# Kernel optimization log

Hardware: AMD Instinct MI355X
Metric: run time of the kernel (lower is better)

## Reference

```python
import jax, jax.numpy as jnp
import numpy as np

N_QUBITS = 10
N_LAYERS = 4
DIM = 2 ** N_QUBITS


def _bit(v, q, n):
    return (v >> (n - 1 - q)) & 1


def _cnot_indices(control, target, n):
    idx0, idx1 = [], []
    for i in range(2 ** n):
        if _bit(i, control, n) == 1 and _bit(i, target, n) == 0:
            idx0.append(i)
            idx1.append(i | (1 << (n - 1 - target)))
    return np.asarray(idx0, np.int32), np.asarray(idx1, np.int32)


# static precomputed CNOT swap indices for pairs (q, (q+1) % n)
_CNOT = [_cnot_indices(q, (q + 1) % N_QUBITS, N_QUBITS) for q in range(N_QUBITS)]
# Z expectation masks: [n_qubits, dim] of +/-1
_ZMASK = np.array([[1.0 - 2.0 * _bit(i, q, N_QUBITS) for i in range(DIM)]
                   for q in range(N_QUBITS)], np.float32)


def _rx(t):
    c = jnp.cos(t / 2.0).astype(jnp.complex64)
    s = jnp.sin(t / 2.0).astype(jnp.complex64)
    return jnp.stack([jnp.stack([c, -1j * s], -1),
                      jnp.stack([-1j * s, c], -1)], -2)


def _ry(t):
    c = jnp.cos(t / 2.0).astype(jnp.complex64)
    s = jnp.sin(t / 2.0).astype(jnp.complex64)
    return jnp.stack([jnp.stack([c, -s], -1),
                      jnp.stack([s, c], -1)], -2)


def _rz(t):
    tc = t.astype(jnp.complex64)
    e0 = jnp.exp(-1j * tc / 2.0)
    e1 = jnp.exp(1j * tc / 2.0)
    z = jnp.zeros_like(e0)
    return jnp.stack([jnp.stack([e0, z], -1),
                      jnp.stack([z, e1], -1)], -2)


def _apply_gate(state, gate, q):
    # state: [b, DIM] complex64; gate: [2,2] or [b,2,2]
    b = state.shape[0]
    psi = state.reshape((b,) + (2,) * N_QUBITS)
    psi = jnp.moveaxis(psi, q + 1, N_QUBITS).reshape(b, DIM // 2, 2)
    if gate.ndim == 3:
        out = jnp.einsum('bmi,bij->bmj', psi, gate)
    else:
        out = jnp.einsum('bmi,ij->bmj', psi, gate)
    out = out.reshape((b,) + (2,) * N_QUBITS)
    out = jnp.moveaxis(out, N_QUBITS, q + 1)
    return out.reshape(b, DIM)


def _cnot(state, idx0, idx1):
    return state.at[:, idx0].set(state[:, idx1]).at[:, idx1].set(state[:, idx0])


def setup_inputs() -> dict:
    key = jax.random.key(0)
    k1, k2, k3, k4 = jax.random.split(key, 4)
    x = jax.random.normal(k1, (16384, 3), jnp.float32)
    enc_W = jax.random.normal(k2, (N_QUBITS, 3), jnp.float32) * 0.3
    enc_b = jax.random.normal(k3, (N_QUBITS,), jnp.float32) * 0.1
    theta = jax.random.normal(k4, (N_LAYERS, N_QUBITS, 3), jnp.float32) * 0.04
    return {"x": x, "enc_W": enc_W, "enc_b": enc_b, "theta": theta}


def reference(x, enc_W, enc_b, theta):
    b = x.shape[0]
    enc = jnp.pi * jnp.tanh(x @ enc_W.T + enc_b)  # [b, n_qubits]
    state = jnp.zeros((b, DIM), jnp.complex64).at[:, 0].set(1.0 + 0j)
    # batched encoding RY rotations
    for q in range(N_QUBITS):
        state = _apply_gate(state, _ry(enc[:, q]), q)
    # variational layers (shared gate across batch)
    for layer in range(N_LAYERS):
        for q in range(N_QUBITS):
            state = _apply_gate(state, _rx(theta[layer, q, 0]), q)
            state = _apply_gate(state, _ry(theta[layer, q, 1]), q)
            state = _apply_gate(state, _rz(theta[layer, q, 2]), q)
        for idx0, idx1 in _CNOT:
            state = _cnot(state, idx0, idx1)
    probs = jnp.square(state.real) + jnp.square(state.imag)  # [b, DIM]
    return probs @ jnp.asarray(_ZMASK).T  # [b, n_qubits]
```

## Files before the change

### kernel.cpp

```cpp
#include <hip/hip_runtime.h>
#include <stdint.h>

#define NQ 10
#define NL 4

typedef unsigned int u32;
typedef _Float16 f16x8 __attribute__((ext_vector_type(8)));
typedef float f32x16 __attribute__((ext_vector_type(16)));
typedef u32 u32x4 __attribute__((ext_vector_type(4)));

constexpr u32 FRc(u32 r) {
    u32 r0 = r & 1, r1 = (r >> 1) & 1, r2 = (r >> 2) & 1, r3 = (r >> 3) & 1, r4 = (r >> 4) & 1;
    return (r4 << 9) | ((r3 ^ r4) << 8) | ((r2 ^ r3) << 7) | ((r1 ^ r2) << 6) |
           ((r0 ^ r1) << 5) | (r0 << 4);
}
constexpr u32 FCc(u32 c) {
    u32 c0 = c & 1, c1 = (c >> 1) & 1, c2 = (c >> 2) & 1, c3 = (c >> 3) & 1, c4 = (c >> 4) & 1;
    return (c0 << 9) | (c0 << 8) | (c4 << 4) | ((c3 ^ c4) << 3) | ((c2 ^ c3) << 2) |
           ((c1 ^ c2) << 1) | (c0 ^ c1);
}
constexpr u32 FIr(u32 r) {
    u32 r0 = r & 1, r1 = (r >> 1) & 1, r2 = (r >> 2) & 1, r3 = (r >> 3) & 1, r4 = (r >> 4) & 1;
    u32 P = r0 ^ r1 ^ r2 ^ r3 ^ r4;
    return ((r0 ^ r1 ^ r2 ^ r3) << 9) | ((r3 ^ r4) << 8) | ((r2 ^ r3 ^ r4) << 7) |
           ((r1 ^ r2 ^ r3 ^ r4) << 6) | (P << 5) | (P << 4) | (P << 3) | (P << 2) | (P << 1) | P;
}
constexpr u32 FIcf(u32 c) {
    u32 c0 = c & 1, c1 = (c >> 1) & 1, c2 = (c >> 2) & 1, c3 = (c >> 3) & 1, c4 = (c >> 4) & 1;
    u32 Q = c0 ^ c1 ^ c2 ^ c3 ^ c4;
    return (Q << 9) | (c4 << 4) | ((c3 ^ c4) << 3) | ((c2 ^ c3 ^ c4) << 2) |
           ((c1 ^ c2 ^ c3 ^ c4) << 1) | Q;
}

__device__ __forceinline__ f32x16 mfma16(f16x8 a, f16x8 b, f32x16 c) {
    return __builtin_amdgcn_mfma_f32_32x32x16_f16(a, b, c, 0, 0, 0);
}
__device__ __forceinline__ f32x16 zero16() {
    f32x16 z;
#pragma unroll
    for (int i = 0; i < 16; i++) z[i] = 0.f;
    return z;
}
__device__ __forceinline__ f16x8 negf(f16x8 v) {
    u32x4 u = __builtin_bit_cast(u32x4, v);
#pragma unroll
    for (int i = 0; i < 4; i++) u[i] ^= 0x80008000u;
    return __builtin_bit_cast(f16x8, u);
}
__device__ __forceinline__ u32 pk2(float re, float im) {
    auto h = __builtin_amdgcn_cvt_pkrtz(re, im);
    return __builtin_bit_cast(u32, h);
}
__device__ __forceinline__ u32 permlo(u32 a, u32 b) {
    return __builtin_amdgcn_perm(b, a, 0x05040100u);
}
__device__ __forceinline__ u32 permhi(u32 a, u32 b) {
    return __builtin_amdgcn_perm(b, a, 0x07060302u);
}
__device__ __forceinline__ f16x8 mk8(u32 a, u32 b, u32 c, u32 d) {
    u32x4 v;
    v[0] = a; v[1] = b; v[2] = c; v[3] = d;
    return __builtin_bit_cast(f16x8, v);
}
template <int MASK>
__device__ __forceinline__ float swz(float v) {
    return __int_as_float(
        __builtin_amdgcn_ds_swizzle(__float_as_int(v), (MASK << 10) | 0x1F));
}
__device__ __forceinline__ float bperm(int addr, float v) {
    return __int_as_float(__builtin_amdgcn_ds_bpermute(addr, __float_as_int(v)));
}
__device__ __forceinline__ void cmulh(float ar, float ai, float br, float bi,
                                      float& cr, float& ci) {
    cr = ar * br - ai * bi;
    ci = ar * bi + ai * br;
}

__global__ void tq_prep(const float* __restrict__ theta, uint16_t* __restrict__ frag) {
    __shared__ float g[NL * NQ][8];
    int tt = threadIdx.x;
    if (tt < NL * NQ) {
        float hx = 0.5f * theta[tt * 3 + 0];
        float hy = 0.5f * theta[tt * 3 + 1];
        float hz = 0.5f * theta[tt * 3 + 2];
        float cx = cosf(hx), sx = sinf(hx);
        float cy = cosf(hy), sy = sinf(hy);
        float cz = cosf(hz), sz = sinf(hz);
        float m00r = cx * cy, m00i = -sx * sy;
        float m01r = -cx * sy, m01i = -sx * cy;
        float m10r = cx * sy, m10i = -sx * cy;
        float m11r = cx * cy, m11i = sx * sy;
        float g00r, g00i, g01r, g01i, g10r, g10i, g11r, g11i;
        cmulh(m00r, m00i, cz, -sz, g00r, g00i);
        cmulh(m10r, m10i, cz, -sz, g10r, g10i);
        cmulh(m01r, m01i, cz, sz, g01r, g01i);
        cmulh(m11r, m11i, cz, sz, g11r, g11i);
        g[tt][0] = g00r; g[tt][1] = g00i; g[tt][2] = g01r; g[tt][3] = g01i;
        g[tt][4] = g10r; g[tt][5] = g10i; g[tt][6] = g11r; g[tt][7] = g11i;
    }
    __syncthreads();
    int t = blockIdx.x * blockDim.x + tt;
    int lane = t & 63, kh = (t >> 6) & 1, part = (t >> 7) & 1, mat = (t >> 8) & 1, l = t >> 9;
    int mn = lane & 31, hf = (lane >> 5) & 1;
#pragma unroll
    for (int j = 0; j < 8; j++) {
        int k = kh * 16 + hf * 8 + j;
        float pr = 1.f, pi = 0.f;
#pragma unroll
        for (int u = 0; u < 5; u++) {
            int q = mat ? (5 + u) : u;
            int bi_ = (k >> (4 - u)) & 1;
            int bo_ = (mn >> (4 - u)) & 1;
            const float* gg = g[l * NQ + q];
            float er = gg[(bi_ * 2 + bo_) * 2 + 0];
            float ei = gg[(bi_ * 2 + bo_) * 2 + 1];
            float nr, ni;
            cmulh(pr, pi, er, ei, nr, ni);
            pr = nr;
            pi = ni;
        }
        float v = part ? pi : pr;
        _Float16 h = (_Float16)v;
        frag[t * 8 + j] = __builtin_bit_cast(unsigned short, h);
    }
}

__global__ __launch_bounds__(256) void tq_main(
    const float* __restrict__ x, const float* __restrict__ encW,
    const float* __restrict__ encb, const uint16_t* __restrict__ frag,
    float* __restrict__ out, int batch) {
    __shared__ u32 smem[4 * 1056];
    int tid = threadIdx.x;
    int wave = (blockIdx.x * blockDim.x + tid) >> 6;
    int lane = tid & 63;
    if (wave >= batch) return;
    u32* slab = smem + (tid >> 6) * 1056;
    const int col = lane & 31;
    const int half = lane >> 5;
    const int addr32 = (lane ^ 32) << 2;
    const u32 Fc5 = FCc((u32)col);
    const u32 FIc_l = FIcf((u32)col);

    float x0 = x[wave * 3 + 0], x1 = x[wave * 3 + 1], x2 = x[wave * 3 + 2];
    float hc = 1.f, hs = 0.f;
    if (lane < NQ) {
        float tta = 3.14159265358979323846f *
                    tanhf(x0 * encW[lane * 3 + 0] + x1 * encW[lane * 3 + 1] +
                          x2 * encW[lane * 3 + 2] + encb[lane]);
        float h = 0.5f * tta;
        hc = cosf(h);
        hs = sinf(h);
    }
    float fcv[NQ], fsv[NQ];
#pragma unroll
    for (int q = 0; q < NQ; q++) {
        fcv[q] = __shfl(hc, q, 64);
        fsv[q] = __shfl(hs, q, 64);
    }
    float colf = 1.f;
    colf *= ((col >> 4) & 1) ? -fsv[5] : fcv[5];
    colf *= ((col >> 3) & 1) ? -fsv[6] : fcv[6];
    colf *= ((col >> 2) & 1) ? -fsv[7] : fcv[7];
    colf *= ((col >> 1) & 1) ? -fsv[8] : fcv[8];
    colf *= (col & 1) ? -fsv[9] : fcv[9];
    float f1h = half ? -fsv[1] : fcv[1];
    float gj[8];
#pragma unroll
    for (int j = 0; j < 8; j++) {
        gj[j] = ((j & 4) ? -fsv[2] : fcv[2]) * ((j & 2) ? -fsv[3] : fcv[3]) *
                ((j & 1) ? -fsv[4] : fcv[4]);
    }
    f16x8 Sr0, Sr1, Si0, Si1;
#pragma unroll
    for (int j = 0; j < 8; j++) {
        Sr0[j] = (_Float16)(fcv[0] * f1h * gj[j] * colf);
        Sr1[j] = (_Float16)(-fsv[0] * f1h * gj[j] * colf);
        Si0[j] = (_Float16)0.f;
        Si1[j] = (_Float16)0.f;
    }

    const f16x8* fr = (const f16x8*)frag;
#define FRAG(l, mat, part, kh) fr[(((((l)*2 + (mat)) * 2 + (part)) * 2 + (kh)) * 64) + lane]

    f32x16 Ur, Ui;
#pragma unroll
    for (int l = 0; l < NL; l++) {
        f16x8 Wr0 = FRAG(l, 0, 0, 0), Wr1 = FRAG(l, 0, 0, 1);
        f16x8 Wi0 = FRAG(l, 0, 1, 0), Wi1 = FRAG(l, 0, 1, 1);
        f16x8 Vr0 = FRAG(l, 1, 0, 0), Vr1 = FRAG(l, 1, 0, 1);
        f16x8 Vi0 = FRAG(l, 1, 1, 0), Vi1 = FRAG(l, 1, 1, 1);

        f32x16 Tr = zero16(), Ti = zero16();
        Tr = mfma16(Wr0, Sr0, Tr);
        Tr = mfma16(Wr1, Sr1, Tr);
        Ti = mfma16(Wi0, Sr0, Ti);
        Ti = mfma16(Wi1, Sr1, Ti);
        if (l > 0) {
            f16x8 nSi0 = negf(Si0), nSi1 = negf(Si1);
            Tr = mfma16(Wi0, nSi0, Tr);
            Tr = mfma16(Wi1, nSi1, Tr);
            Ti = mfma16(Wr0, Si0, Ti);
            Ti = mfma16(Wr1, Si1, Ti);
        }

        {
            u32* wb = slab + col + half * (4 * 33);
#pragma unroll
            for (int gi = 0; gi < 16; gi++) {
                int rb = (gi & 3) + 8 * (gi >> 2);
                wb[rb * 33] = pk2(Tr[gi], Ti[gi]);
            }
        }
        u32 ta[16];
        {
            u32* rb = slab + col * 33 + half * 8;
#pragma unroll
            for (int kh = 0; kh < 2; kh++)
#pragma unroll
                for (int j = 0; j < 8; j++) ta[kh * 8 + j] = rb[kh * 16 + j];
        }
        f16x8 TAr0 = mk8(permlo(ta[0], ta[1]), permlo(ta[2], ta[3]),
                         permlo(ta[4], ta[5]), permlo(ta[6], ta[7]));
        f16x8 TAr1 = mk8(permlo(ta[8], ta[9]), permlo(ta[10], ta[11]),
                         permlo(ta[12], ta[13]), permlo(ta[14], ta[15]));
        f16x8 TAi0 = mk8(permhi(ta[0], ta[1]), permhi(ta[2], ta[3]),
                         permhi(ta[4], ta[5]), permhi(ta[6], ta[7]));
        f16x8 TAi1 = mk8(permhi(ta[8], ta[9]), permhi(ta[10], ta[11]),
                         permhi(ta[12], ta[13]), permhi(ta[14], ta[15]));

        Ur = zero16();
        Ui = zero16();
        Ur = mfma16(TAr0, Vr0, Ur);
        Ur = mfma16(TAr1, Vr1, Ur);
        {
            f16x8 nTAi0 = negf(TAi0), nTAi1 = negf(TAi1);
            Ur = mfma16(nTAi0, Vi0, Ur);
            Ur = mfma16(nTAi1, Vi1, Ur);
        }
        Ui = mfma16(TAr0, Vi0, Ui);
        Ui = mfma16(TAr1, Vi1, Ui);
        Ui = mfma16(TAi0, Vr0, Ui);
        Ui = mfma16(TAi1, Vr1, Ui);

        if (l < NL - 1) {
            {
                u32* wb = slab + col + half * (4 * 32);
#pragma unroll
                for (int gi = 0; gi < 16; gi++) {
                    int rb = (gi & 3) + 8 * (gi >> 2);
                    wb[rb * 32] = pk2(Ur[gi], Ui[gi]);
                }
            }
            u32 sb[16];
            {
                u32 fh = Fc5 ^ (half ? FRc(8) : 0u);
#pragma unroll
                for (int kh = 0; kh < 2; kh++)
#pragma unroll
                    for (int j = 0; j < 8; j++)
                        sb[kh * 8 + j] = slab[FRc(kh * 16 + j) ^ fh];
            }
            Sr0 = mk8(permlo(sb[0], sb[1]), permlo(sb[2], sb[3]),
                      permlo(sb[4], sb[5]), permlo(sb[6], sb[7]));
            Sr1 = mk8(permlo(sb[8], sb[9]), permlo(sb[10], sb[11]),
                      permlo(sb[12], sb[13]), permlo(sb[14], sb[15]));
            Si0 = mk8(permhi(sb[0], sb[1]), permhi(sb[2], sb[3]),
                      permhi(sb[4], sb[5]), permhi(sb[6], sb[7]));
            Si1 = mk8(permhi(sb[8], sb[9]), permhi(sb[10], sb[11]),
                      permhi(sb[12], sb[13]), permhi(sb[14], sb[15]));
        }
    }

    float acc[NQ];
#pragma unroll
    for (int q = 0; q < NQ; q++) acc[q] = 0.f;
#pragma unroll
    for (int gi = 0; gi < 16; gi++) {
        int rb = (gi & 3) + 8 * (gi >> 2);
        u32 minv = FIr((u32)rb) ^ (half ? FIr(4) : 0u) ^ FIc_l;
        float p = Ur[gi] * Ur[gi] + Ui[gi] * Ui[gi];
        float np = -p;
#pragma unroll
        for (int q = 0; q < NQ; q++) acc[q] += ((minv >> (9 - q)) & 1) ? np : p;
    }
#pragma unroll
    for (int q = 0; q < NQ; q++) {
        float v = acc[q];
        v += swz<1>(v);
        v += swz<2>(v);
        v += swz<4>(v);
        v += swz<8>(v);
        v += swz<16>(v);
        v += bperm(addr32, v);
        acc[q] = v;
    }
    float o = acc[0];
#pragma unroll
    for (int q = 1; q < NQ; q++) o = (lane == q) ? acc[q] : o;
    if (lane < NQ) out[wave * NQ + lane] = o;
}

extern "C" void kernel_launch(void* const* d_in, const int* in_sizes, int n_in,
                              void* d_out, int out_size, void* d_ws, size_t ws_size,
                              hipStream_t stream) {
    const float* x = (const float*)d_in[0];
    const float* encW = (const float*)d_in[1];
    const float* encb = (const float*)d_in[2];
    const float* th = (const float*)d_in[3];
    float* out = (float*)d_out;
    uint16_t* frag = (uint16_t*)d_ws;
    int batch = in_sizes[0] / 3;

    tq_prep<<<2, 1024, 0, stream>>>(th, frag);
    int total_threads = batch * 64;
    tq_main<<<(total_threads + 255) / 256, 256, 0, stream>>>(x, encW, encb, frag, out, batch);
}
```

Before: 112.1 us.

## Fuse gate-fragment prep into main kernel and replace LDS transposes with bpermute

Removes the separate prep kernel: each block rebuilds the per-layer gate fragments in shared memory, using a factored 4-qubit-plus-1 Kronecker build. It swaps operand order in the first MFMA stage so that the intermediate transpose becomes a cross-half ds_bpermute exchange instead of an LDS round trip. The final Z-expectation reduction now runs as an MFMA against a +/-1 sign matrix, which shrinks the per-qubit shuffle reductions. In exchange every block redoes the fragment computation (trig and products), and per-block shared memory grows to about 52 KB, which may limit occupancy.

```diff
diff --git a/kernel.cpp b/kernel.cpp
--- a/kernel.cpp
+++ b/kernel.cpp
@@ -19,18 +19,6 @@
     return (c0 << 9) | (c0 << 8) | (c4 << 4) | ((c3 ^ c4) << 3) | ((c2 ^ c3) << 2) |
            ((c1 ^ c2) << 1) | (c0 ^ c1);
 }
-constexpr u32 FIr(u32 r) {
-    u32 r0 = r & 1, r1 = (r >> 1) & 1, r2 = (r >> 2) & 1, r3 = (r >> 3) & 1, r4 = (r >> 4) & 1;
-    u32 P = r0 ^ r1 ^ r2 ^ r3 ^ r4;
-    return ((r0 ^ r1 ^ r2 ^ r3) << 9) | ((r3 ^ r4) << 8) | ((r2 ^ r3 ^ r4) << 7) |
-           ((r1 ^ r2 ^ r3 ^ r4) << 6) | (P << 5) | (P << 4) | (P << 3) | (P << 2) | (P << 1) | P;
-}
-constexpr u32 FIcf(u32 c) {
-    u32 c0 = c & 1, c1 = (c >> 1) & 1, c2 = (c >> 2) & 1, c3 = (c >> 3) & 1, c4 = (c >> 4) & 1;
-    u32 Q = c0 ^ c1 ^ c2 ^ c3 ^ c4;
-    return (Q << 9) | (c4 << 4) | ((c3 ^ c4) << 3) | ((c2 ^ c3 ^ c4) << 2) |
-           ((c1 ^ c2 ^ c3 ^ c4) << 1) | Q;
-}
 
 __device__ __forceinline__ f32x16 mfma16(f16x8 a, f16x8 b, f32x16 c) {
     return __builtin_amdgcn_mfma_f32_32x32x16_f16(a, b, c, 0, 0, 0);
@@ -47,42 +35,57 @@
     for (int i = 0; i < 4; i++) u[i] ^= 0x80008000u;
     return __builtin_bit_cast(f16x8, u);
 }
-__device__ __forceinline__ u32 pk2(float re, float im) {
-    auto h = __builtin_amdgcn_cvt_pkrtz(re, im);
+__device__ __forceinline__ u32 pk2(float a, float b) {
+    auto h = __builtin_amdgcn_cvt_pkrtz(a, b);
     return __builtin_bit_cast(u32, h);
 }
-__device__ __forceinline__ u32 permlo(u32 a, u32 b) {
-    return __builtin_amdgcn_perm(b, a, 0x05040100u);
-}
-__device__ __forceinline__ u32 permhi(u32 a, u32 b) {
-    return __builtin_amdgcn_perm(b, a, 0x07060302u);
-}
+__device__ __forceinline__ u32 permlo(u32 a, u32 b) { return __builtin_amdgcn_perm(b, a, 0x05040100u); }
+__device__ __forceinline__ u32 permhi(u32 a, u32 b) { return __builtin_amdgcn_perm(b, a, 0x07060302u); }
 __device__ __forceinline__ f16x8 mk8(u32 a, u32 b, u32 c, u32 d) {
-    u32x4 v;
-    v[0] = a; v[1] = b; v[2] = c; v[3] = d;
+    u32x4 v; v[0] = a; v[1] = b; v[2] = c; v[3] = d;
     return __builtin_bit_cast(f16x8, v);
 }
 template <int MASK>
 __device__ __forceinline__ float swz(float v) {
-    return __int_as_float(
-        __builtin_amdgcn_ds_swizzle(__float_as_int(v), (MASK << 10) | 0x1F));
-}
-__device__ __forceinline__ float bperm(int addr, float v) {
-    return __int_as_float(__builtin_amdgcn_ds_bpermute(addr, __float_as_int(v)));
-}
-__device__ __forceinline__ void cmulh(float ar, float ai, float br, float bi,
-                                      float& cr, float& ci) {
+    return __int_as_float(__builtin_amdgcn_ds_swizzle(__float_as_int(v), (MASK << 10) | 0x1F));
+}
+__device__ __forceinline__ u32 bpermu(int addr, u32 v) {
+    return (u32)__builtin_amdgcn_ds_bpermute(addr, (int)v);
+}
+__device__ __forceinline__ void cmulh(float ar, float ai, float br, float bi, float& cr, float& ci) {
     cr = ar * br - ai * bi;
     ci = ar * bi + ai * br;
 }
 
-__global__ void tq_prep(const float* __restrict__ theta, uint16_t* __restrict__ frag) {
-    __shared__ float g[NL * NQ][8];
-    int tt = threadIdx.x;
-    if (tt < NL * NQ) {
-        float hx = 0.5f * theta[tt * 3 + 0];
-        float hy = 0.5f * theta[tt * 3 + 1];
-        float hz = 0.5f * theta[tt * 3 + 2];
+__device__ __forceinline__ void c2a(const f32x16& V, bool hb, int addr32, u32 (&o)[8]) {
+    u32 pw[8];
+#pragma unroll
+    for (int p = 0; p < 8; p++) pw[p] = pk2(V[2 * p], V[2 * p + 1]);
+    u32 s0 = hb ? pw[0] : pw[2];
+    u32 s1 = hb ? pw[1] : pw[3];
+    u32 s2 = hb ? pw[4] : pw[6];
+    u32 s3 = hb ? pw[5] : pw[7];
+    u32 r0 = bpermu(addr32, s0), r1 = bpermu(addr32, s1);
+    u32 r2 = bpermu(addr32, s2), r3 = bpermu(addr32, s3);
+    o[0] = hb ? r0 : pw[0]; o[1] = hb ? r1 : pw[1];
+    o[2] = hb ? pw[2] : r0; o[3] = hb ? pw[3] : r1;
+    o[4] = hb ? r2 : pw[4]; o[5] = hb ? r3 : pw[5];
+    o[6] = hb ? pw[6] : r2; o[7] = hb ? pw[7] : r3;
+}
+
+__global__ __launch_bounds__(256) void tq_all(
+    const float* __restrict__ x, const float* __restrict__ encW,
+    const float* __restrict__ encb, const float* __restrict__ theta,
+    float* __restrict__ out, int batch) {
+    __shared__ u32 pool[13120];
+    const int tid = threadIdx.x;
+    float* gp = (float*)(pool + 12800);
+    float2* K4p = (float2*)(pool + 8704);
+
+    if (tid < NL * NQ) {
+        float hx = 0.5f * theta[tid * 3 + 0];
+        float hy = 0.5f * theta[tid * 3 + 1];
+        float hz = 0.5f * theta[tid * 3 + 2];
         float cx = cosf(hx), sx = sinf(hx);
         float cy = cosf(hy), sy = sinf(hy);
         float cz = cosf(hz), sz = sinf(hz);
@@ -95,51 +98,85 @@
         cmulh(m10r, m10i, cz, -sz, g10r, g10i);
         cmulh(m01r, m01i, cz, sz, g01r, g01i);
         cmulh(m11r, m11i, cz, sz, g11r, g11i);
-        g[tt][0] = g00r; g[tt][1] = g00i; g[tt][2] = g01r; g[tt][3] = g01i;
-        g[tt][4] = g10r; g[tt][5] = g10i; g[tt][6] = g11r; g[tt][7] = g11i;
+        float* o = gp + tid * 8;
+        o[0] = g00r; o[1] = g00i; o[2] = g01r; o[3] = g01i;
+        o[4] = g10r; o[5] = g10i; o[6] = g11r; o[7] = g11i;
+    }
+    if (tid < 128) {
+        int lane = tid & 63, kh = tid >> 6;
+        int q = lane & 31, hf = (lane >> 5) & 1;
+        u32 M = (q == 0) ? 0xFu : (q == 1) ? 0x18u : (q == 2) ? 0x1Cu : (q == 3) ? 0x1Eu : 0x1Fu;
+        u32 w[4];
+#pragma unroll
+        for (int p = 0; p < 4; p++) {
+            int k0 = kh * 16 + hf * 8 + 2 * p, k1 = k0 + 1;
+            float v0 = (__builtin_popcount((u32)k0 & M) & 1) ? -1.f : 1.f;
+            float v1 = (__builtin_popcount((u32)k1 & M) & 1) ? -1.f : 1.f;
+            w[p] = pk2(v0, v1);
+        }
+        u32x4 v4; v4[0] = w[0]; v4[1] = w[1]; v4[2] = w[2]; v4[3] = w[3];
+        *(u32x4*)(pool + (32 + kh) * 256 + lane * 4) = v4;
     }
     __syncthreads();
-    int t = blockIdx.x * blockDim.x + tt;
-    int lane = t & 63, kh = (t >> 6) & 1, part = (t >> 7) & 1, mat = (t >> 8) & 1, l = t >> 9;
-    int mn = lane & 31, hf = (lane >> 5) & 1;
-#pragma unroll
-    for (int j = 0; j < 8; j++) {
-        int k = kh * 16 + hf * 8 + j;
+#pragma unroll 1
+    for (int rr = 0; rr < 8; rr++) {
+        int e = rr * 256 + tid;
+        int lm = e >> 8, idx = e & 255, k = idx >> 4, m = idx & 15;
+        int gb = (lm >> 1) * 10 + (lm & 1) * 5;
         float pr = 1.f, pi = 0.f;
 #pragma unroll
-        for (int u = 0; u < 5; u++) {
-            int q = mat ? (5 + u) : u;
-            int bi_ = (k >> (4 - u)) & 1;
-            int bo_ = (mn >> (4 - u)) & 1;
-            const float* gg = g[l * NQ + q];
-            float er = gg[(bi_ * 2 + bo_) * 2 + 0];
-            float ei = gg[(bi_ * 2 + bo_) * 2 + 1];
+        for (int u = 0; u < 4; u++) {
+            const float* gg = gp + (gb + u) * 8;
+            int bi = (k >> (3 - u)) & 1, bo = (m >> (3 - u)) & 1;
+            float er = gg[(bi * 2 + bo) * 2 + 0], ei = gg[(bi * 2 + bo) * 2 + 1];
             float nr, ni;
             cmulh(pr, pi, er, ei, nr, ni);
-            pr = nr;
-            pi = ni;
-        }
-        float v = part ? pi : pr;
-        _Float16 h = (_Float16)v;
-        frag[t * 8 + j] = __builtin_bit_cast(unsigned short, h);
-    }
-}
-
-__global__ __launch_bounds__(256) void tq_main(
-    const float* __restrict__ x, const float* __restrict__ encW,
-    const float* __restrict__ encb, const uint16_t* __restrict__ frag,
-    float* __restrict__ out, int batch) {
-    __shared__ u32 smem[4 * 1056];
-    int tid = threadIdx.x;
-    int wave = (blockIdx.x * blockDim.x + tid) >> 6;
+            pr = nr; pi = ni;
+        }
+        K4p[lm * 256 + idx] = make_float2(pr, pi);
+    }
+    __syncthreads();
+#pragma unroll 1
+    for (int rr = 0; rr < 4; rr++) {
+        int t = rr * 256 + tid;
+        int lane = t & 63, kh = (t >> 6) & 1, lm = t >> 7;
+        int m = lane & 31, hf = (lane >> 5) & 1;
+        int gb = (lm >> 1) * 10 + (lm & 1) * 5;
+        const float* g4 = gp + (gb + 4) * 8;
+        int mu = m & 1;
+        float e0r = g4[mu * 2 + 0], e0i = g4[mu * 2 + 1];
+        float e1r = g4[(2 + mu) * 2 + 0], e1i = g4[(2 + mu) * 2 + 1];
+        float2 kv[4];
+#pragma unroll
+        for (int jj = 0; jj < 4; jj++)
+            kv[jj] = K4p[lm * 256 + (kh * 8 + hf * 4 + jj) * 16 + (m >> 1)];
+        float vr[8], vi[8];
+#pragma unroll
+        for (int j = 0; j < 8; j++) {
+            float2 a = kv[j >> 1];
+            float er = (j & 1) ? e1r : e0r, ei = (j & 1) ? e1i : e0i;
+            cmulh(a.x, a.y, er, ei, vr[j], vi[j]);
+        }
+        u32x4 wre, wim;
+#pragma unroll
+        for (int p = 0; p < 4; p++) {
+            wre[p] = pk2(vr[2 * p], vr[2 * p + 1]);
+            wim[p] = pk2(vi[2 * p], vi[2 * p + 1]);
+        }
+        *(u32x4*)(pool + (lm * 4 + kh) * 256 + lane * 4) = wre;
+        *(u32x4*)(pool + (lm * 4 + 2 + kh) * 256 + lane * 4) = wim;
+    }
+    __syncthreads();
+
+    int wave = blockIdx.x * 4 + (tid >> 6);
     int lane = tid & 63;
     if (wave >= batch) return;
-    u32* slab = smem + (tid >> 6) * 1056;
+    u32* slab = pool + 8704 + (tid >> 6) * 1024;
     const int col = lane & 31;
-    const int half = lane >> 5;
+    const int half_ = lane >> 5;
+    const bool hb = half_ != 0;
     const int addr32 = (lane ^ 32) << 2;
     const u32 Fc5 = FCc((u32)col);
-    const u32 FIc_l = FIcf((u32)col);
 
     float x0 = x[wave * 3 + 0], x1 = x[wave * 3 + 1], x2 = x[wave * 3 + 2];
     float hc = 1.f, hs = 0.f;
@@ -163,7 +200,7 @@
     colf *= ((col >> 2) & 1) ? -fsv[7] : fcv[7];
     colf *= ((col >> 1) & 1) ? -fsv[8] : fcv[8];
     colf *= (col & 1) ? -fsv[9] : fcv[9];
-    float f1h = half ? -fsv[1] : fcv[1];
+    float f1h = half_ ? -fsv[1] : fcv[1];
     float gj[8];
 #pragma unroll
     for (int j = 0; j < 8; j++) {
@@ -179,54 +216,35 @@
         Si1[j] = (_Float16)0.f;
     }
 
-    const f16x8* fr = (const f16x8*)frag;
-#define FRAG(l, mat, part, kh) fr[(((((l)*2 + (mat)) * 2 + (part)) * 2 + (kh)) * 64) + lane]
-
+    const f16x8* FR = (const f16x8*)pool;
     f32x16 Ur, Ui;
 #pragma unroll
     for (int l = 0; l < NL; l++) {
-        f16x8 Wr0 = FRAG(l, 0, 0, 0), Wr1 = FRAG(l, 0, 0, 1);
-        f16x8 Wi0 = FRAG(l, 0, 1, 0), Wi1 = FRAG(l, 0, 1, 1);
-        f16x8 Vr0 = FRAG(l, 1, 0, 0), Vr1 = FRAG(l, 1, 0, 1);
-        f16x8 Vi0 = FRAG(l, 1, 1, 0), Vi1 = FRAG(l, 1, 1, 1);
+        f16x8 Wr0 = FR[(8 * l + 0) * 64 + lane], Wr1 = FR[(8 * l + 1) * 64 + lane];
+        f16x8 Wi0 = FR[(8 * l + 2) * 64 + lane], Wi1 = FR[(8 * l + 3) * 64 + lane];
+        f16x8 Vr0 = FR[(8 * l + 4) * 64 + lane], Vr1 = FR[(8 * l + 5) * 64 + lane];
+        f16x8 Vi0 = FR[(8 * l + 6) * 64 + lane], Vi1 = FR[(8 * l + 7) * 64 + lane];
 
         f32x16 Tr = zero16(), Ti = zero16();
-        Tr = mfma16(Wr0, Sr0, Tr);
-        Tr = mfma16(Wr1, Sr1, Tr);
-        Ti = mfma16(Wi0, Sr0, Ti);
-        Ti = mfma16(Wi1, Sr1, Ti);
+        Tr = mfma16(Sr0, Wr0, Tr);
+        Tr = mfma16(Sr1, Wr1, Tr);
+        Ti = mfma16(Sr0, Wi0, Ti);
+        Ti = mfma16(Sr1, Wi1, Ti);
         if (l > 0) {
             f16x8 nSi0 = negf(Si0), nSi1 = negf(Si1);
-            Tr = mfma16(Wi0, nSi0, Tr);
-            Tr = mfma16(Wi1, nSi1, Tr);
-            Ti = mfma16(Wr0, Si0, Ti);
-            Ti = mfma16(Wr1, Si1, Ti);
-        }
-
-        {
-            u32* wb = slab + col + half * (4 * 33);
-#pragma unroll
-            for (int gi = 0; gi < 16; gi++) {
-                int rb = (gi & 3) + 8 * (gi >> 2);
-                wb[rb * 33] = pk2(Tr[gi], Ti[gi]);
-            }
-        }
-        u32 ta[16];
-        {
-            u32* rb = slab + col * 33 + half * 8;
-#pragma unroll
-            for (int kh = 0; kh < 2; kh++)
-#pragma unroll
-                for (int j = 0; j < 8; j++) ta[kh * 8 + j] = rb[kh * 16 + j];
-        }
-        f16x8 TAr0 = mk8(permlo(ta[0], ta[1]), permlo(ta[2], ta[3]),
-                         permlo(ta[4], ta[5]), permlo(ta[6], ta[7]));
-        f16x8 TAr1 = mk8(permlo(ta[8], ta[9]), permlo(ta[10], ta[11]),
-                         permlo(ta[12], ta[13]), permlo(ta[14], ta[15]));
-        f16x8 TAi0 = mk8(permhi(ta[0], ta[1]), permhi(ta[2], ta[3]),
-                         permhi(ta[4], ta[5]), permhi(ta[6], ta[7]));
-        f16x8 TAi1 = mk8(permhi(ta[8], ta[9]), permhi(ta[10], ta[11]),
-                         permhi(ta[12], ta[13]), permhi(ta[14], ta[15]));
+            Tr = mfma16(nSi0, Wi0, Tr);
+            Tr = mfma16(nSi1, Wi1, Tr);
+            Ti = mfma16(Si0, Wr0, Ti);
+            Ti = mfma16(Si1, Wr1, Ti);
+        }
+
+        u32 oR[8], oI[8];
+        c2a(Tr, hb, addr32, oR);
+        c2a(Ti, hb, addr32, oI);
+        f16x8 TAr0 = mk8(oR[0], oR[1], oR[2], oR[3]);
+        f16x8 TAr1 = mk8(oR[4], oR[5], oR[6], oR[7]);
+        f16x8 TAi0 = mk8(oI[0], oI[1], oI[2], oI[3]);
+        f16x8 TAi1 = mk8(oI[4], oI[5], oI[6], oI[7]);
 
         Ur = zero16();
         Ui = zero16();
@@ -244,7 +262,7 @@
 
         if (l < NL - 1) {
             {
-                u32* wb = slab + col + half * (4 * 32);
+                u32* wb = slab + col + half_ * (4 * 32);
 #pragma unroll
                 for (int gi = 0; gi < 16; gi++) {
                     int rb = (gi & 3) + 8 * (gi >> 2);
@@ -253,7 +271,7 @@
             }
             u32 sb[16];
             {
-                u32 fh = Fc5 ^ (half ? FRc(8) : 0u);
+                u32 fh = Fc5 ^ (half_ ? FRc(8) : 0u);
 #pragma unroll
                 for (int kh = 0; kh < 2; kh++)
 #pragma unroll
@@ -271,33 +289,46 @@
         }
     }
 
-    float acc[NQ];
-#pragma unroll
-    for (int q = 0; q < NQ; q++) acc[q] = 0.f;
-#pragma unroll
-    for (int gi = 0; gi < 16; gi++) {
-        int rb = (gi & 3) + 8 * (gi >> 2);
-        u32 minv = FIr((u32)rb) ^ (half ? FIr(4) : 0u) ^ FIc_l;
-        float p = Ur[gi] * Ur[gi] + Ui[gi] * Ui[gi];
-        float np = -p;
-#pragma unroll
-        for (int q = 0; q < NQ; q++) acc[q] += ((minv >> (9 - q)) & 1) ? np : p;
-    }
-#pragma unroll
-    for (int q = 0; q < NQ; q++) {
-        float v = acc[q];
+    f32x16 P;
+#pragma unroll
+    for (int gi = 0; gi < 16; gi++) P[gi] = Ur[gi] * Ur[gi] + Ui[gi] * Ui[gi];
+    u32 po[8];
+    c2a(P, hb, addr32, po);
+    f16x8 PB0 = mk8(po[0], po[1], po[2], po[3]);
+    f16x8 PB1 = mk8(po[4], po[5], po[6], po[7]);
+    f16x8 Srw0 = FR[32 * 64 + lane], Srw1 = FR[33 * 64 + lane];
+    f32x16 D = mfma16(Srw0, PB0, mfma16(Srw1, PB1, zero16()));
+
+    u32 b4 = (col >> 4) & 1, b3 = (col >> 3) & 1, b2 = (col >> 2) & 1,
+        b1 = (col >> 1) & 1, b0 = col & 1;
+    u32 p4 = b4, p43 = p4 ^ b3, p432 = p43 ^ b2, p4321 = p432 ^ b1, pall = p4321 ^ b0;
+    u32 sg[6];
+    sg[0] = hb ? 0u : pall;
+    sg[1] = hb ? p4 : 0u;
+    sg[2] = hb ? p43 : 0u;
+    sg[3] = hb ? p432 : 0u;
+    sg[4] = hb ? 0u : p4321;
+    sg[5] = hb ? 0u : pall;
+    float red[6];
+#pragma unroll
+    for (int s = 0; s < 6; s++) {
+        float v = __uint_as_float(__float_as_uint(D[s]) ^ (sg[s] << 31));
         v += swz<1>(v);
         v += swz<2>(v);
         v += swz<4>(v);
         v += swz<8>(v);
         v += swz<16>(v);
-        v += bperm(addr32, v);
-        acc[q] = v;
-    }
-    float o = acc[0];
-#pragma unroll
-    for (int q = 1; q < NQ; q++) o = (lane == q) ? acc[q] : o;
-    if (lane < NQ) out[wave * NQ + lane] = o;
+        red[s] = v;
+    }
+    int cc = col - ((col >= 4) ? 4 : 0);
+    float v = red[0];
+    v = (cc == 1) ? red[1] : v;
+    v = (cc == 2) ? red[2] : v;
+    v = (cc == 3) ? red[3] : v;
+    v = (cc == 4) ? red[4] : v;
+    v = (cc == 5) ? red[5] : v;
+    bool st = hb ? (col >= 4 && col < 8) : (col < 4 || col == 8 || col == 9);
+    if (st) out[wave * NQ + col] = v;
 }
 
 extern "C" void kernel_launch(void* const* d_in, const int* in_sizes, int n_in,
@@ -308,10 +339,7 @@
     const float* encb = (const float*)d_in[2];
     const float* th = (const float*)d_in[3];
     float* out = (float*)d_out;
-    uint16_t* frag = (uint16_t*)d_ws;
     int batch = in_sizes[0] / 3;
-
-    tq_prep<<<2, 1024, 0, stream>>>(th, frag);
-    int total_threads = batch * 64;
-    tq_main<<<(total_threads + 255) / 256, 256, 0, stream>>>(x, encW, encb, frag, out, batch);
-}
+    int blocks = (batch + 3) / 4;
+    tq_all<<<blocks, 256, 0, stream>>>(x, encW, encb, th, out, batch);
+}
```

After: 113.7 us. Within noise of the previous version (+1.5%).
